# Optimization experiments

Measured on AMD Instinct MI355X. Metric: run time of the kernel, lower is better.

The kernel has to match this reference:

```python
import jax, jax.numpy as jnp
import numpy as np

N_NODES = 50000
N_EDGES = 800000
IN_CH = 256
HID = 256
OUT_CH = 128


def setup_inputs() -> dict:
    key = jax.random.key(0)
    ks = jax.random.split(key, 12)
    x = jax.random.normal(ks[0], (N_NODES, IN_CH), dtype=jnp.float32)
    adj_rows = jnp.sort(jax.random.randint(ks[1], (N_EDGES,), 0, N_NODES, dtype=jnp.int32))
    adj_cols = jax.random.randint(ks[2], (N_EDGES,), 0, N_NODES, dtype=jnp.int32)
    # normalized adjacency weights (~1/degree scale)
    adj_vals = jax.random.uniform(ks[3], (N_EDGES,), dtype=jnp.float32) / 16.0
    def xavier(k, fan_in, fan_out):
        lim = float(np.sqrt(6.0 / (fan_in + fan_out)))
        return jax.random.uniform(k, (fan_in, fan_out), dtype=jnp.float32, minval=-lim, maxval=lim)
    Wa0 = xavier(ks[4], IN_CH, HID)
    Wa1 = xavier(ks[5], HID, HID)
    Wl0 = xavier(ks[6], IN_CH + HID, HID)
    Wl1 = xavier(ks[7], 2 * HID, OUT_CH)
    return {
        'x': x, 'adj_rows': adj_rows, 'adj_cols': adj_cols, 'adj_vals': adj_vals,
        'Wa0': Wa0, 'ba0': jnp.zeros((HID,), jnp.float32),
        'Wa1': Wa1, 'ba1': jnp.zeros((HID,), jnp.float32),
        'Wl0': Wl0, 'bl0': jnp.zeros((HID,), jnp.float32),
        'Wl1': Wl1, 'bl1': jnp.zeros((OUT_CH,), jnp.float32),
    }


def reference(x, adj_rows, adj_cols, adj_vals, Wa0, ba0, Wa1, ba1, Wl0, bl0, Wl1, bl1):
    n = x.shape[0]

    def spmm(h):
        # sparse adj @ h : gather neighbor rows, scale by edge weight, segment-sum into dst
        return jax.ops.segment_sum(adj_vals[:, None] * h[adj_cols], adj_rows, num_segments=n)

    # layer 0
    agg = jax.nn.relu(spmm(x) @ Wa0 + ba0)
    h = jax.nn.relu(jnp.concatenate((x, agg), axis=1) @ Wl0 + bl0)
    # layer 1 (last: no activation after linear)
    agg = jax.nn.relu(spmm(h) @ Wa1 + ba1)
    h = jnp.concatenate((h, agg), axis=1) @ Wl1 + bl1
    # F.normalize: row-wise L2 with eps=1e-12
    norm = jnp.maximum(jnp.linalg.norm(h, axis=1, keepdims=True), 1e-12)
    return h / norm
```

## Files before the change

kernel.cpp:

```cpp
#include <hip/hip_runtime.h>

typedef unsigned short u16;
typedef __attribute__((ext_vector_type(8))) __bf16 bf16x8;
typedef __attribute__((ext_vector_type(4))) float f32x4;
typedef __attribute__((ext_vector_type(8))) u16 u16x8;
typedef __attribute__((ext_vector_type(4))) u16 u16x4;

__device__ __forceinline__ float bf2f(u16 u) {
  return __builtin_bit_cast(float, ((unsigned)u) << 16);
}
__device__ __forceinline__ u16 f2bf(float f) {
  unsigned x = __builtin_bit_cast(unsigned, f);
  x += 0x7fffu + ((x >> 16) & 1u);
  return (u16)(x >> 16);
}
__device__ __forceinline__ f32x4 cvt4(u16x4 v) {
  return (f32x4){bf2f(v.x), bf2f(v.y), bf2f(v.z), bf2f(v.w)};
}
__device__ __forceinline__ void gload_lds16(const void* g, void* l) {
  __builtin_amdgcn_global_load_lds(
      (const __attribute__((address_space(1))) void*)g,
      (__attribute__((address_space(3))) void*)l, 16, 0, 0);
}

__global__ void prep_kernel(const float* __restrict__ x, u16* __restrict__ x_bf, int cvtxBlocks,
                            const float* __restrict__ W0, u16* __restrict__ T0,
                            const float* __restrict__ W1, u16* __restrict__ T1,
                            const float* __restrict__ W2, u16* __restrict__ T2,
                            const float* __restrict__ W3, u16* __restrict__ T3,
                            const int* __restrict__ rows, int nE, int* __restrict__ rp, int nN) {
  int b = blockIdx.x;
  if (b < cvtxBlocks) {
    int i = b * 256 + threadIdx.x;
    if (i >= nN * 64) return;
    const float4 v = ((const float4*)x)[i];
    u16x4 o = { f2bf(v.x), f2bf(v.y), f2bf(v.z), f2bf(v.w) };
    ((u16x4*)x_bf)[i] = o;
    return;
  }
  b -= cvtxBlocks;
  if (b < 1280) {
    int i = b * 256 + threadIdx.x;
    const float* W; u16* T; int K, N;
    if (i < 65536)        { W = W0; T = T0; K = 256; N = 256; }
    else if (i < 131072)  { W = W1; T = T1; K = 256; N = 256; i -= 65536; }
    else if (i < 262144)  { W = W2; T = T2; K = 512; N = 256; i -= 131072; }
    else if (i < 327680)  { W = W3; T = T3; K = 512; N = 128; i -= 262144; }
    else return;
    int k = i / N, n = i - k * N;
    T[(size_t)n * K + k] = f2bf(W[i]);
    return;
  }
  b -= 1280;
  int i = b * 256 + threadIdx.x;
  if (i > nN) return;
  int lo = 0, hi = nE;
  while (lo < hi) { int mid = (lo + hi) >> 1; if (rows[mid] < i) lo = mid + 1; else hi = mid; }
  rp[i] = lo;
}

__global__ __launch_bounds__(128) void spmm_kernel(
    const u16* __restrict__ X, const int* __restrict__ rp,
    const int* __restrict__ cols, const float* __restrict__ vals,
    u16* __restrict__ out, int nN) {
  int lane = threadIdx.x & 63;
  int node = blockIdx.x * 2 + (threadIdx.x >> 6);
  if (node >= nN) return;
  int e0 = rp[node], e1 = rp[node + 1];
  f32x4 s0 = {0.f, 0.f, 0.f, 0.f}, s1 = s0, s2 = s0, s3 = s0;
  const u16* xp = X + (size_t)lane * 4;
  int e = e0;
  for (; e + 8 <= e1; e += 8) {
    int c[8]; float v[8]; u16x4 xv[8];
    #pragma unroll
    for (int i = 0; i < 8; ++i) { c[i] = cols[e + i]; v[i] = vals[e + i]; }
    #pragma unroll
    for (int i = 0; i < 8; ++i) xv[i] = *(const u16x4*)(xp + (size_t)c[i] * 256);
    s0 += v[0] * cvt4(xv[0]); s1 += v[1] * cvt4(xv[1]);
    s2 += v[2] * cvt4(xv[2]); s3 += v[3] * cvt4(xv[3]);
    s0 += v[4] * cvt4(xv[4]); s1 += v[5] * cvt4(xv[5]);
    s2 += v[6] * cvt4(xv[6]); s3 += v[7] * cvt4(xv[7]);
  }
  if (e + 4 <= e1) {
    int c0 = cols[e], c1 = cols[e + 1], c2 = cols[e + 2], c3 = cols[e + 3];
    float v0 = vals[e], v1 = vals[e + 1], v2 = vals[e + 2], v3 = vals[e + 3];
    u16x4 x0 = *(const u16x4*)(xp + (size_t)c0 * 256);
    u16x4 x1 = *(const u16x4*)(xp + (size_t)c1 * 256);
    u16x4 x2 = *(const u16x4*)(xp + (size_t)c2 * 256);
    u16x4 x3 = *(const u16x4*)(xp + (size_t)c3 * 256);
    s0 += v0 * cvt4(x0); s1 += v1 * cvt4(x1);
    s2 += v2 * cvt4(x2); s3 += v3 * cvt4(x3);
    e += 4;
  }
  for (; e < e1; ++e) {
    int c = cols[e];
    float v = vals[e];
    s0 += v * cvt4(*(const u16x4*)(xp + (size_t)c * 256));
  }
  f32x4 s = (s0 + s1) + (s2 + s3);
  u16x4 o = { f2bf(s.x), f2bf(s.y), f2bf(s.z), f2bf(s.w) };
  *(u16x4*)(out + (size_t)node * 256 + lane * 4) = o;
}

template<int KTOT, bool SPLIT, bool RELU, bool OUTF32, bool NORM, int NB>
__global__ __launch_bounds__(256) void gemm_kernel(
    const u16* __restrict__ A0, const u16* __restrict__ A1,
    const u16* __restrict__ Wt, const float* __restrict__ bias,
    void* __restrict__ outp, int M, int N) {
  __shared__ u16 As[2][64 * 64];
  __shared__ u16 Bs[2][128 * 64];
  __shared__ float red[64][2];

  const int lane = threadIdx.x & 63;
  const int wid = threadIdx.x >> 6;
  const int wr = wid >> 1, wc = wid & 1;

  int row0b, col0b;
  if (NB == 2) {
    const int b = blockIdx.x;
    const int g = b >> 4, w = b & 15;
    const int nfull = gridDim.x >> 4;
    int pair, col;
    if (g < nfull) { pair = g * 8 + (w & 7); col = w >> 3; }
    else { int rem = b - (nfull << 4); pair = nfull * 8 + (rem >> 1); col = rem & 1; }
    row0b = pair * 64; col0b = col * 128;
  } else {
    row0b = blockIdx.x * 64; col0b = 0;
  }

  const int lr = lane & 15;
  const int kg = lane >> 4;

  auto stage = [&](int buf, int kt) {
    const u16* Asrc = (!SPLIT || kt < 4) ? A0 : A1;
    const int kkl = (!SPLIT || kt < 4) ? kt * 64 : (kt - 4) * 64;
    #pragma unroll
    for (int i = 0; i < 2; ++i) {
      const int ca = wid * 2 + i;
      const int uu = ca * 64 + lane;
      const int row = uu >> 3;
      const int kss = (uu & 7) ^ (row & 7);
      int grow = row0b + row;
      if (grow >= M) grow = M - 1;
      gload_lds16(Asrc + (size_t)grow * 256 + kkl + kss * 8, &As[buf][ca * 512]);
    }
    #pragma unroll
    for (int i = 0; i < 4; ++i) {
      const int cb = wid * 4 + i;
      const int uu = cb * 64 + lane;
      const int row = uu >> 3;
      const int kss = (uu & 7) ^ (row & 7);
      gload_lds16(Wt + (size_t)(col0b + row) * KTOT + kt * 64 + kss * 8, &Bs[buf][cb * 512]);
    }
  };

  f32x4 acc[2][4];
  #pragma unroll
  for (int ni = 0; ni < 4; ++ni) {
    float bv = bias[col0b + wc * 64 + ni * 16 + lr];
    #pragma unroll
    for (int mi = 0; mi < 2; ++mi) acc[mi][ni] = (f32x4){bv, bv, bv, bv};
  }

  constexpr int KSTEPS = KTOT / 64;
  stage(0, 0);
  __syncthreads();

  for (int kt = 0; kt < KSTEPS; ++kt) {
    const int cur = kt & 1;
    if (kt + 1 < KSTEPS) stage(cur ^ 1, kt + 1);

    #pragma unroll
    for (int ks = 0; ks < 2; ++ks) {
      const int q = ks * 4 + kg;
      bf16x8 a[2], b[4];
      #pragma unroll
      for (int mi = 0; mi < 2; ++mi) {
        const int r = wr * 32 + mi * 16 + lr;
        a[mi] = __builtin_bit_cast(bf16x8,
            *(const u16x8*)&As[cur][r * 64 + (q ^ (r & 7)) * 8]);
      }
      #pragma unroll
      for (int ni = 0; ni < 4; ++ni) {
        const int cb = wc * 64 + ni * 16 + lr;
        b[ni] = __builtin_bit_cast(bf16x8,
            *(const u16x8*)&Bs[cur][cb * 64 + (q ^ (cb & 7)) * 8]);
      }
      #pragma unroll
      for (int mi = 0; mi < 2; ++mi)
        #pragma unroll
        for (int ni = 0; ni < 4; ++ni)
          acc[mi][ni] = __builtin_amdgcn_mfma_f32_16x16x32_bf16(a[mi], b[ni], acc[mi][ni], 0, 0, 0);
    }
    __syncthreads();
  }

  float invn[2][4];
  if (NORM) {
    #pragma unroll
    for (int mi = 0; mi < 2; ++mi) {
      #pragma unroll
      for (int j = 0; j < 4; ++j) {
        float p = 0.f;
        #pragma unroll
        for (int ni = 0; ni < 4; ++ni) { float v = acc[mi][ni][j]; p += v * v; }
        #pragma unroll
        for (int m = 1; m < 16; m <<= 1) p += __shfl_xor(p, m, 64);
        int rl = wr * 32 + mi * 16 + kg * 4 + j;
        if (lr == 0) red[rl][wc] = p;
        invn[mi][j] = 0.f;
      }
    }
    __syncthreads();
    #pragma unroll
    for (int mi = 0; mi < 2; ++mi) {
      #pragma unroll
      for (int j = 0; j < 4; ++j) {
        int rl = wr * 32 + mi * 16 + kg * 4 + j;
        float ss = red[rl][0] + red[rl][1];
        float nrm = sqrtf(ss);
        nrm = nrm > 1e-12f ? nrm : 1e-12f;
        invn[mi][j] = 1.f / nrm;
      }
    }
  }

  #pragma unroll
  for (int mi = 0; mi < 2; ++mi) {
    #pragma unroll
    for (int j = 0; j < 4; ++j) {
      int r = row0b + wr * 32 + mi * 16 + kg * 4 + j;
      if (r >= M) continue;
      #pragma unroll
      for (int ni = 0; ni < 4; ++ni) {
        float v = acc[mi][ni][j];
        if (RELU) v = v > 0.f ? v : 0.f;
        if (NORM) v *= invn[mi][j];
        int c = col0b + wc * 64 + ni * 16 + lr;
        if (OUTF32) ((float*)outp)[(size_t)r * N + c] = v;
        else        ((u16*)outp)[(size_t)r * N + c] = f2bf(v);
      }
    }
  }
}

extern "C" void kernel_launch(void* const* d_in, const int* in_sizes, int n_in,
                              void* d_out, int out_size, void* d_ws, size_t ws_size,
                              hipStream_t stream) {
  const float* x        = (const float*)d_in[0];
  const int*   adj_rows = (const int*)d_in[1];
  const int*   adj_cols = (const int*)d_in[2];
  const float* adj_vals = (const float*)d_in[3];
  const float* Wa0 = (const float*)d_in[4];
  const float* ba0 = (const float*)d_in[5];
  const float* Wa1 = (const float*)d_in[6];
  const float* ba1 = (const float*)d_in[7];
  const float* Wl0 = (const float*)d_in[8];
  const float* bl0 = (const float*)d_in[9];
  const float* Wl1 = (const float*)d_in[10];
  const float* bl1 = (const float*)d_in[11];

  const int nN = in_sizes[0] / 256;
  const int nE = in_sizes[1];

  char* ws = (char*)d_ws;
  size_t off = 0;
  auto alloc = [&](size_t bytes) -> void* {
    void* p = ws + off;
    off += (bytes + 255) & ~(size_t)255;
    return p;
  };
  u16* x_bf  = (u16*)alloc((size_t)nN * 256 * 2);
  u16* aggA  = (u16*)alloc((size_t)nN * 256 * 2);
  u16* aggB  = (u16*)alloc((size_t)nN * 256 * 2);
  u16* h_bf  = (u16*)alloc((size_t)nN * 256 * 2);
  int* rp    = (int*)alloc((size_t)(nN + 1) * 4);
  u16* wt_a0 = (u16*)alloc(256 * 256 * 2);
  u16* wt_a1 = (u16*)alloc(256 * 256 * 2);
  u16* wt_l0 = (u16*)alloc(512 * 256 * 2);
  u16* wt_l1 = (u16*)alloc(512 * 128 * 2);
  if (off > ws_size) return;

  dim3 blk(256);
  const int cvtxBlocks = (nN * 64 + 255) / 256;
  const int rpBlocks = (nN + 1 + 255) / 256;
  prep_kernel<<<dim3(cvtxBlocks + 1280 + rpBlocks), blk, 0, stream>>>(
      x, x_bf, cvtxBlocks, Wa0, wt_a0, Wa1, wt_a1, Wl0, wt_l0, Wl1, wt_l1,
      adj_rows, nE, rp, nN);

  const int MB = (nN + 63) / 64;
  dim3 gN256(2 * MB);
  dim3 gN128(MB);
  dim3 gNode((nN + 1) / 2);
  dim3 sblk(128);

  spmm_kernel<<<gNode, sblk, 0, stream>>>(x_bf, rp, adj_cols, adj_vals, aggA, nN);
  gemm_kernel<256, false, true, false, false, 2><<<gN256, blk, 0, stream>>>(aggA, nullptr, wt_a0, ba0, aggB, nN, 256);
  gemm_kernel<512, true, true, false, false, 2><<<gN256, blk, 0, stream>>>(x_bf, aggB, wt_l0, bl0, h_bf, nN, 256);
  spmm_kernel<<<gNode, sblk, 0, stream>>>(h_bf, rp, adj_cols, adj_vals, aggA, nN);
  gemm_kernel<256, false, true, false, false, 2><<<gN256, blk, 0, stream>>>(aggA, nullptr, wt_a1, ba1, aggB, nN, 256);
  gemm_kernel<512, true, false, true, true, 1><<<gN128, blk, 0, stream>>>(h_bf, aggB, wt_l1, bl1, (float*)d_out, nN, 128);
}
```

Before: 221.7 us.

## Fuse aggregation GEMM and concat-linear GEMM into one kernel per layer

Each layer's two back-to-back GEMMs are merged into one kernel. The ReLU'd aggregation output for a 64-row tile stays in a swizzled LDS buffer and feeds the second GEMM's second half of K directly. This removes the aggB intermediate round trip through global memory and two kernel launches. Weight operands are now read straight from global memory (through cache) instead of being staged in LDS. Each block also covers the full 256-wide output, so there are fewer blocks and more accumulator registers and LDS per block, which may lower occupancy.

```diff
diff --git a/kernel.cpp b/kernel.cpp
--- a/kernel.cpp
+++ b/kernel.cpp
@@ -102,118 +102,157 @@
   *(u16x4*)(out + (size_t)node * 256 + lane * 4) = o;
 }
 
-template<int KTOT, bool SPLIT, bool RELU, bool OUTF32, bool NORM, int NB>
-__global__ __launch_bounds__(256) void gemm_kernel(
-    const u16* __restrict__ A0, const u16* __restrict__ A1,
-    const u16* __restrict__ Wt, const float* __restrict__ bias,
-    void* __restrict__ outp, int M, int N) {
+template<int N2, bool NORM>
+__global__ __launch_bounds__(256) void fused_kernel(
+    const u16* __restrict__ agg, const u16* __restrict__ xh,
+    const u16* __restrict__ W1t, const float* __restrict__ b1,
+    const u16* __restrict__ W2t, const float* __restrict__ b2,
+    void* __restrict__ outp, int M) {
+  constexpr int NI2 = N2 / 32;
   __shared__ u16 As[2][64 * 64];
-  __shared__ u16 Bs[2][128 * 64];
+  __shared__ u16 Ag[64 * 256];
   __shared__ float red[64][2];
 
   const int lane = threadIdx.x & 63;
   const int wid = threadIdx.x >> 6;
   const int wr = wid >> 1, wc = wid & 1;
-
-  int row0b, col0b;
-  if (NB == 2) {
-    const int b = blockIdx.x;
-    const int g = b >> 4, w = b & 15;
-    const int nfull = gridDim.x >> 4;
-    int pair, col;
-    if (g < nfull) { pair = g * 8 + (w & 7); col = w >> 3; }
-    else { int rem = b - (nfull << 4); pair = nfull * 8 + (rem >> 1); col = rem & 1; }
-    row0b = pair * 64; col0b = col * 128;
-  } else {
-    row0b = blockIdx.x * 64; col0b = 0;
-  }
-
-  const int lr = lane & 15;
-  const int kg = lane >> 4;
-
-  auto stage = [&](int buf, int kt) {
-    const u16* Asrc = (!SPLIT || kt < 4) ? A0 : A1;
-    const int kkl = (!SPLIT || kt < 4) ? kt * 64 : (kt - 4) * 64;
+  const int row0b = blockIdx.x * 64;
+  const int lr = lane & 15, kg = lane >> 4;
+
+  auto stageA = [&](int buf, const u16* src, int kt) {
     #pragma unroll
     for (int i = 0; i < 2; ++i) {
-      const int ca = wid * 2 + i;
-      const int uu = ca * 64 + lane;
-      const int row = uu >> 3;
-      const int kss = (uu & 7) ^ (row & 7);
-      int grow = row0b + row;
-      if (grow >= M) grow = M - 1;
-      gload_lds16(Asrc + (size_t)grow * 256 + kkl + kss * 8, &As[buf][ca * 512]);
-    }
-    #pragma unroll
-    for (int i = 0; i < 4; ++i) {
-      const int cb = wid * 4 + i;
-      const int uu = cb * 64 + lane;
-      const int row = uu >> 3;
-      const int kss = (uu & 7) ^ (row & 7);
-      gload_lds16(Wt + (size_t)(col0b + row) * KTOT + kt * 64 + kss * 8, &Bs[buf][cb * 512]);
+      const int u = (wid * 2 + i) * 64 + lane;
+      const int row = u >> 3;
+      const int kss = (u & 7) ^ (row & 7);
+      int grow = row0b + row; if (grow >= M) grow = M - 1;
+      gload_lds16(src + (size_t)grow * 256 + kt * 64 + kss * 8, &As[buf][u * 8]);
     }
   };
 
-  f32x4 acc[2][4];
-  #pragma unroll
-  for (int ni = 0; ni < 4; ++ni) {
-    float bv = bias[col0b + wc * 64 + ni * 16 + lr];
-    #pragma unroll
-    for (int mi = 0; mi < 2; ++mi) acc[mi][ni] = (f32x4){bv, bv, bv, bv};
-  }
-
-  constexpr int KSTEPS = KTOT / 64;
-  stage(0, 0);
+  f32x4 acc[2][8];
+
+  #pragma unroll
+  for (int ni = 0; ni < 8; ++ni) {
+    float bv = b1[wc * 128 + ni * 16 + lr];
+    acc[0][ni] = (f32x4){bv, bv, bv, bv};
+    acc[1][ni] = acc[0][ni];
+  }
+  stageA(0, agg, 0);
   __syncthreads();
-
-  for (int kt = 0; kt < KSTEPS; ++kt) {
+  for (int kt = 0; kt < 4; ++kt) {
     const int cur = kt & 1;
-    if (kt + 1 < KSTEPS) stage(cur ^ 1, kt + 1);
-
+    if (kt < 3) stageA(cur ^ 1, agg, kt + 1);
     #pragma unroll
     for (int ks = 0; ks < 2; ++ks) {
       const int q = ks * 4 + kg;
-      bf16x8 a[2], b[4];
+      bf16x8 a[2], b[8];
       #pragma unroll
       for (int mi = 0; mi < 2; ++mi) {
         const int r = wr * 32 + mi * 16 + lr;
         a[mi] = __builtin_bit_cast(bf16x8,
-            *(const u16x8*)&As[cur][r * 64 + (q ^ (r & 7)) * 8]);
-      }
-      #pragma unroll
-      for (int ni = 0; ni < 4; ++ni) {
-        const int cb = wc * 64 + ni * 16 + lr;
+            *(const u16x8*)&As[cur][r * 64 + ((q ^ (r & 7)) * 8)]);
+      }
+      #pragma unroll
+      for (int ni = 0; ni < 8; ++ni)
         b[ni] = __builtin_bit_cast(bf16x8,
-            *(const u16x8*)&Bs[cur][cb * 64 + (q ^ (cb & 7)) * 8]);
-      }
+            *(const u16x8*)(W1t + (size_t)(wc * 128 + ni * 16 + lr) * 256 + kt * 64 + q * 8));
       #pragma unroll
       for (int mi = 0; mi < 2; ++mi)
         #pragma unroll
-        for (int ni = 0; ni < 4; ++ni)
+        for (int ni = 0; ni < 8; ++ni)
           acc[mi][ni] = __builtin_amdgcn_mfma_f32_16x16x32_bf16(a[mi], b[ni], acc[mi][ni], 0, 0, 0);
     }
     __syncthreads();
+  }
+  #pragma unroll
+  for (int mi = 0; mi < 2; ++mi)
+    #pragma unroll
+    for (int j = 0; j < 4; ++j) {
+      const int rl = wr * 32 + mi * 16 + kg * 4 + j;
+      #pragma unroll
+      for (int ni = 0; ni < 8; ++ni) {
+        float v = acc[mi][ni][j];
+        v = v > 0.f ? v : 0.f;
+        const int c = wc * 128 + ni * 16 + lr;
+        Ag[rl * 256 + (c >> 6) * 64 + ((((c >> 3) & 7) ^ (rl & 7)) * 8) + (c & 7)] = f2bf(v);
+      }
+    }
+
+  #pragma unroll
+  for (int ni = 0; ni < NI2; ++ni) {
+    float bv = b2[wc * (N2 / 2) + ni * 16 + lr];
+    acc[0][ni] = (f32x4){bv, bv, bv, bv};
+    acc[1][ni] = acc[0][ni];
+  }
+  stageA(0, xh, 0);
+  __syncthreads();
+  for (int kt = 0; kt < 4; ++kt) {
+    const int cur = kt & 1;
+    if (kt < 3) stageA(cur ^ 1, xh, kt + 1);
+    #pragma unroll
+    for (int ks = 0; ks < 2; ++ks) {
+      const int q = ks * 4 + kg;
+      bf16x8 a[2], b[NI2];
+      #pragma unroll
+      for (int mi = 0; mi < 2; ++mi) {
+        const int r = wr * 32 + mi * 16 + lr;
+        a[mi] = __builtin_bit_cast(bf16x8,
+            *(const u16x8*)&As[cur][r * 64 + ((q ^ (r & 7)) * 8)]);
+      }
+      #pragma unroll
+      for (int ni = 0; ni < NI2; ++ni)
+        b[ni] = __builtin_bit_cast(bf16x8,
+            *(const u16x8*)(W2t + (size_t)(wc * (N2 / 2) + ni * 16 + lr) * 512 + kt * 64 + q * 8));
+      #pragma unroll
+      for (int mi = 0; mi < 2; ++mi)
+        #pragma unroll
+        for (int ni = 0; ni < NI2; ++ni)
+          acc[mi][ni] = __builtin_amdgcn_mfma_f32_16x16x32_bf16(a[mi], b[ni], acc[mi][ni], 0, 0, 0);
+    }
+    if (kt < 3) __syncthreads();
+  }
+  #pragma unroll
+  for (int w = 0; w < 4; ++w) {
+    #pragma unroll
+    for (int ks = 0; ks < 2; ++ks) {
+      const int q = ks * 4 + kg;
+      bf16x8 a[2], b[NI2];
+      #pragma unroll
+      for (int mi = 0; mi < 2; ++mi) {
+        const int r = wr * 32 + mi * 16 + lr;
+        a[mi] = __builtin_bit_cast(bf16x8,
+            *(const u16x8*)&Ag[r * 256 + w * 64 + ((q ^ (r & 7)) * 8)]);
+      }
+      #pragma unroll
+      for (int ni = 0; ni < NI2; ++ni)
+        b[ni] = __builtin_bit_cast(bf16x8,
+            *(const u16x8*)(W2t + (size_t)(wc * (N2 / 2) + ni * 16 + lr) * 512 + 256 + w * 64 + q * 8));
+      #pragma unroll
+      for (int mi = 0; mi < 2; ++mi)
+        #pragma unroll
+        for (int ni = 0; ni < NI2; ++ni)
+          acc[mi][ni] = __builtin_amdgcn_mfma_f32_16x16x32_bf16(a[mi], b[ni], acc[mi][ni], 0, 0, 0);
+    }
   }
 
   float invn[2][4];
   if (NORM) {
     #pragma unroll
-    for (int mi = 0; mi < 2; ++mi) {
+    for (int mi = 0; mi < 2; ++mi)
       #pragma unroll
       for (int j = 0; j < 4; ++j) {
         float p = 0.f;
         #pragma unroll
-        for (int ni = 0; ni < 4; ++ni) { float v = acc[mi][ni][j]; p += v * v; }
+        for (int ni = 0; ni < NI2; ++ni) { float v = acc[mi][ni][j]; p += v * v; }
         #pragma unroll
         for (int m = 1; m < 16; m <<= 1) p += __shfl_xor(p, m, 64);
         int rl = wr * 32 + mi * 16 + kg * 4 + j;
         if (lr == 0) red[rl][wc] = p;
-        invn[mi][j] = 0.f;
-      }
-    }
+      }
     __syncthreads();
     #pragma unroll
-    for (int mi = 0; mi < 2; ++mi) {
+    for (int mi = 0; mi < 2; ++mi)
       #pragma unroll
       for (int j = 0; j < 4; ++j) {
         int rl = wr * 32 + mi * 16 + kg * 4 + j;
@@ -222,26 +261,26 @@
         nrm = nrm > 1e-12f ? nrm : 1e-12f;
         invn[mi][j] = 1.f / nrm;
       }
-    }
-  }
-
-  #pragma unroll
-  for (int mi = 0; mi < 2; ++mi) {
+  }
+
+  #pragma unroll
+  for (int mi = 0; mi < 2; ++mi)
     #pragma unroll
     for (int j = 0; j < 4; ++j) {
       int r = row0b + wr * 32 + mi * 16 + kg * 4 + j;
       if (r >= M) continue;
       #pragma unroll
-      for (int ni = 0; ni < 4; ++ni) {
+      for (int ni = 0; ni < NI2; ++ni) {
         float v = acc[mi][ni][j];
-        if (RELU) v = v > 0.f ? v : 0.f;
-        if (NORM) v *= invn[mi][j];
-        int c = col0b + wc * 64 + ni * 16 + lr;
-        if (OUTF32) ((float*)outp)[(size_t)r * N + c] = v;
-        else        ((u16*)outp)[(size_t)r * N + c] = f2bf(v);
-      }
-    }
-  }
+        int c = wc * (N2 / 2) + ni * 16 + lr;
+        if (NORM) {
+          ((float*)outp)[(size_t)r * N2 + c] = v * invn[mi][j];
+        } else {
+          v = v > 0.f ? v : 0.f;
+          ((u16*)outp)[(size_t)r * N2 + c] = f2bf(v);
+        }
+      }
+    }
 }
 
 extern "C" void kernel_launch(void* const* d_in, const int* in_sizes, int n_in,
@@ -272,7 +311,6 @@
   };
   u16* x_bf  = (u16*)alloc((size_t)nN * 256 * 2);
   u16* aggA  = (u16*)alloc((size_t)nN * 256 * 2);
-  u16* aggB  = (u16*)alloc((size_t)nN * 256 * 2);
   u16* h_bf  = (u16*)alloc((size_t)nN * 256 * 2);
   int* rp    = (int*)alloc((size_t)(nN + 1) * 4);
   u16* wt_a0 = (u16*)alloc(256 * 256 * 2);
@@ -289,15 +327,12 @@
       adj_rows, nE, rp, nN);
 
   const int MB = (nN + 63) / 64;
-  dim3 gN256(2 * MB);
-  dim3 gN128(MB);
+  dim3 gF(MB);
   dim3 gNode((nN + 1) / 2);
   dim3 sblk(128);
 
   spmm_kernel<<<gNode, sblk, 0, stream>>>(x_bf, rp, adj_cols, adj_vals, aggA, nN);
-  gemm_kernel<256, false, true, false, false, 2><<<gN256, blk, 0, stream>>>(aggA, nullptr, wt_a0, ba0, aggB, nN, 256);
-  gemm_kernel<512, true, true, false, false, 2><<<gN256, blk, 0, stream>>>(x_bf, aggB, wt_l0, bl0, h_bf, nN, 256);
+  fused_kernel<256, false><<<gF, blk, 0, stream>>>(aggA, x_bf, wt_a0, ba0, wt_l0, bl0, h_bf, nN);
   spmm_kernel<<<gNode, sblk, 0, stream>>>(h_bf, rp, adj_cols, adj_vals, aggA, nN);
-  gemm_kernel<256, false, true, false, false, 2><<<gN256, blk, 0, stream>>>(aggA, nullptr, wt_a1, ba1, aggB, nN, 256);
-  gemm_kernel<512, true, false, true, true, 1><<<gN128, blk, 0, stream>>>(h_bf, aggB, wt_l1, bl1, (float*)d_out, nN, 128);
-}
+  fused_kernel<128, true><<<gF, blk, 0, stream>>>(aggA, h_bf, wt_a1, ba1, wt_l1, bl1, (float*)d_out, nN);
+}
```

After: 296.6 us. 33.8% more time.
